# Performance work log

Hardware: AMD Instinct MI355X
Metric: run time of the kernel (lower is better)

Reference implementation:

```python
import jax, jax.numpy as jnp
import numpy as np

MAX_REL = 2  # hard-coded max_relative_position in the torch module


def setup_inputs() -> dict:
    key = jax.random.key(0)
    ks = jax.random.split(key, 12)
    B, S, Dm, H = 2, 2048, 1024, 16
    D = Dm // H
    sc = 1.0 / np.sqrt(Dm)
    inp = {
        "x": jax.random.normal(ks[0], (B, S, Dm), jnp.float32),
        "Wq": jax.random.normal(ks[1], (Dm, Dm), jnp.float32) * sc,
        "bq": jnp.zeros((Dm,), jnp.float32),
        "Wk": jax.random.normal(ks[2], (Dm, Dm), jnp.float32) * sc,
        "bk": jnp.zeros((Dm,), jnp.float32),
        "Wv": jax.random.normal(ks[3], (Dm, Dm), jnp.float32) * sc,
        "bv": jnp.zeros((Dm,), jnp.float32),
        "Wo": jax.random.normal(ks[4], (Dm, Dm), jnp.float32) * sc,
        "bo": jnp.zeros((Dm,), jnp.float32),
        "rel_k": jax.random.normal(ks[5], (2 * MAX_REL + 1, D), jnp.float32) * 0.1,
        "rel_v": jax.random.normal(ks[6], (2 * MAX_REL + 1, D), jnp.float32) * 0.1,
        "num_heads": H,
    }
    return inp


def reference(x, Wq, bq, Wk, bk, Wv, bv, Wo, bo, rel_k, rel_v, num_heads):
    B, S, Dm = x.shape
    H = num_heads
    D = Dm // H
    n_buckets = 2 * MAX_REL + 1

    q = (x @ Wq + bq).reshape(B, S, H, D).transpose(0, 2, 1, 3)  # [B,H,S,D]
    k = (x @ Wk + bk).reshape(B, S, H, D).transpose(0, 2, 1, 3)
    v = (x @ Wv + bv).reshape(B, S, H, D).transpose(0, 2, 1, 3)

    # content-content scores
    attn1 = jnp.einsum('bhqd,bhkd->bhqk', q, k)

    # relative-position bucket index: clip(k - q, -MAX_REL, MAX_REL) + MAX_REL
    r = jnp.arange(S)
    idx = jnp.clip(r[None, :] - r[:, None], -MAX_REL, MAX_REL) + MAX_REL  # [S,S] int

    # content-position scores: q . rel_k[idx]  (project onto 5 buckets then gather)
    q_rel = jnp.einsum('bhqd,jd->bhqj', q, rel_k)  # [B,H,S,5]
    attn2 = jnp.take_along_axis(q_rel, jnp.broadcast_to(idx[None, None], (B, H, S, S)), axis=-1)

    scores = (attn1 + attn2) / jnp.sqrt(jnp.asarray(D, x.dtype))
    p = jax.nn.softmax(scores, axis=-1)  # dropout in eval mode -> identity

    out1 = jnp.einsum('bhqk,bhkd->bhqd', p, v)

    # position value term: sum_k p[...,k] * rel_v[idx[q,k]] via bucket accumulation
    onehot = (idx[:, :, None] == jnp.arange(n_buckets)[None, None, :]).astype(p.dtype)  # [S,S,5]
    bucket = jnp.einsum('bhqk,qkj->bhqj', p, onehot)
    out2 = jnp.einsum('bhqj,jd->bhqd', bucket, rel_v)

    out = (out1 + out2).transpose(0, 2, 1, 3).reshape(B, S, Dm)
    return out @ Wo + bo
```

## Files before the change

kernel.cpp:

```cpp
#include <hip/hip_runtime.h>

#define S_LEN 2048
#define DM    1024
#define NH    16
#define HD    64
#define BATCH 2

typedef __attribute__((ext_vector_type(8))) short short8;
typedef __attribute__((ext_vector_type(4))) float f32x4;

__device__ inline float b2f(unsigned short u) {
    return __uint_as_float(((unsigned)u) << 16);
}
__device__ inline unsigned short f2b(float f) {
    unsigned u = __float_as_uint(f);
    u += 0x7FFFu + ((u >> 16) & 1u);
    return (unsigned short)(u >> 16);
}
__device__ inline f32x4 zero4() {
    f32x4 z; z[0] = 0.f; z[1] = 0.f; z[2] = 0.f; z[3] = 0.f; return z;
}

__device__ inline size_t qk_frag_idx(int s, int d) {
    return (size_t)(s >> 4) * 1024 + (size_t)(d >> 5) * 512
         + (size_t)(((d & 31) >> 3) * 16 + (s & 15)) * 8 + (d & 7);
}
__device__ inline size_t v_frag_idx(int s, int d) {
    return (size_t)(s >> 5) * 2048 + (size_t)(d >> 4) * 512
         + (size_t)(((s & 31) >> 3) * 16 + (d & 15)) * 8 + (s & 7);
}
__device__ inline size_t af_idx(int m, int k) {
    return ((size_t)(m >> 4) * 32 + (size_t)(k >> 5)) * 512
         + (size_t)(((k & 31) >> 3) * 16 + (m & 15)) * 8 + (k & 7);
}

__global__ __launch_bounds__(256) void convert_w(
    const float* __restrict__ Wq, const float* __restrict__ Wk,
    const float* __restrict__ Wv, const float* __restrict__ Wo,
    unsigned short* __restrict__ Wf)
{
    int k = blockIdx.x, mat = blockIdx.y, tid = threadIdx.x;
    const float* W = (mat == 0) ? Wq : (mat == 1) ? Wk : (mat == 2) ? Wv : Wo;
    f32x4 w = *(const f32x4*)(W + (size_t)k * DM + tid * 4);
    unsigned short* dst = Wf + ((size_t)mat << 20);
#pragma unroll
    for (int e = 0; e < 4; e++) dst[af_idx(tid * 4 + e, k)] = f2b(w[e]);
}

__global__ __launch_bounds__(256) void convert_x(
    const float* __restrict__ x, unsigned short* __restrict__ Xf, int b)
{
    int m = blockIdx.x, tid = threadIdx.x;
    f32x4 v = *(const f32x4*)(x + ((size_t)b * S_LEN + m) * DM + tid * 4);
#pragma unroll
    for (int e = 0; e < 4; e++) Xf[af_idx(m, tid * 4 + e)] = f2b(v[e]);
}

__global__ __launch_bounds__(256) void proj_gemm_wf(
    const unsigned short* __restrict__ Xf,
    const unsigned short* __restrict__ Wf,
    const float* __restrict__ bq, const float* __restrict__ bk,
    const float* __restrict__ bv,
    unsigned short* __restrict__ Qs, unsigned short* __restrict__ Ks,
    unsigned short* __restrict__ Vts)
{
    int tid = threadIdx.x;
    int wave = tid >> 6, lane = tid & 63;
    int r = lane & 15, quad = lane >> 4;
    int mat = blockIdx.y >> 4;
    int hh  = blockIdx.y & 15;

    int mt0 = blockIdx.x * 8 + wave * 2;
    const unsigned short* A0 = Xf + (size_t)mt0 * 32 * 512 + lane * 8;
    const unsigned short* A1 = A0 + 32 * 512;
    const unsigned short* Bb = Wf + ((size_t)mat << 20)
                             + (size_t)(hh * 4) * 32 * 512 + lane * 8;

    f32x4 acc[2][4];
#pragma unroll
    for (int mt = 0; mt < 2; mt++)
#pragma unroll
        for (int nt = 0; nt < 4; nt++) acc[mt][nt] = zero4();

    short8 a0c = *(const short8*)A0;
    short8 a1c = *(const short8*)A1;
    short8 b0c = *(const short8*)(Bb);
    short8 b1c = *(const short8*)(Bb + 16384);
    short8 b2c = *(const short8*)(Bb + 32768);
    short8 b3c = *(const short8*)(Bb + 49152);

    for (int kt = 0; kt < 32; kt++) {
        short8 a0n, a1n, b0n, b1n, b2n, b3n;
        if (kt < 31) {
            size_t off = (size_t)(kt + 1) * 512;
            a0n = *(const short8*)(A0 + off);
            a1n = *(const short8*)(A1 + off);
            b0n = *(const short8*)(Bb + off);
            b1n = *(const short8*)(Bb + 16384 + off);
            b2n = *(const short8*)(Bb + 32768 + off);
            b3n = *(const short8*)(Bb + 49152 + off);
        }
        acc[0][0] = __builtin_amdgcn_mfma_f32_16x16x32_bf16(a0c, b0c, acc[0][0], 0, 0, 0);
        acc[0][1] = __builtin_amdgcn_mfma_f32_16x16x32_bf16(a0c, b1c, acc[0][1], 0, 0, 0);
        acc[0][2] = __builtin_amdgcn_mfma_f32_16x16x32_bf16(a0c, b2c, acc[0][2], 0, 0, 0);
        acc[0][3] = __builtin_amdgcn_mfma_f32_16x16x32_bf16(a0c, b3c, acc[0][3], 0, 0, 0);
        acc[1][0] = __builtin_amdgcn_mfma_f32_16x16x32_bf16(a1c, b0c, acc[1][0], 0, 0, 0);
        acc[1][1] = __builtin_amdgcn_mfma_f32_16x16x32_bf16(a1c, b1c, acc[1][1], 0, 0, 0);
        acc[1][2] = __builtin_amdgcn_mfma_f32_16x16x32_bf16(a1c, b2c, acc[1][2], 0, 0, 0);
        acc[1][3] = __builtin_amdgcn_mfma_f32_16x16x32_bf16(a1c, b3c, acc[1][3], 0, 0, 0);
        a0c = a0n; a1c = a1n;
        b0c = b0n; b1c = b1n; b2c = b2n; b3c = b3n;
    }

    const float* bias = (mat == 0) ? bq : (mat == 1) ? bk : bv;
    size_t hbase = (size_t)hh * S_LEN * HD;
    int gc0 = hh * 64;
#pragma unroll
    for (int mt = 0; mt < 2; mt++) {
#pragma unroll
        for (int nt = 0; nt < 4; nt++) {
            int d = nt * 16 + r;
            float bb = bias[gc0 + d];
#pragma unroll
            for (int i = 0; i < 4; i++) {
                int s = blockIdx.x * 128 + wave * 32 + mt * 16 + quad * 4 + i;
                float v = acc[mt][nt][i] + bb;
                if (mat == 2)      Vts[hbase + v_frag_idx(s, d)] = f2b(v);
                else if (mat == 0) Qs [hbase + qk_frag_idx(s, d)] = f2b(v);
                else               Ks [hbase + qk_frag_idx(s, d)] = f2b(v);
            }
        }
    }
}

__global__ __launch_bounds__(256) void outproj_wf(
    const unsigned short* __restrict__ AOf,
    const unsigned short* __restrict__ Wof,
    const float* __restrict__ bo,
    float* __restrict__ out, int b)
{
    int tid = threadIdx.x;
    int wave = tid >> 6, lane = tid & 63;
    int r = lane & 15, quad = lane >> 4;

    int mt0 = blockIdx.x * 8 + wave * 2;
    const unsigned short* A0 = AOf + (size_t)mt0 * 32 * 512 + lane * 8;
    const unsigned short* A1 = A0 + 32 * 512;
    const unsigned short* Bb = Wof + (size_t)(blockIdx.y * 4) * 32 * 512 + lane * 8;

    f32x4 acc[2][4];
#pragma unroll
    for (int mt = 0; mt < 2; mt++)
#pragma unroll
        for (int nt = 0; nt < 4; nt++) acc[mt][nt] = zero4();

    short8 a0c = *(const short8*)A0;
    short8 a1c = *(const short8*)A1;
    short8 b0c = *(const short8*)(Bb);
    short8 b1c = *(const short8*)(Bb + 16384);
    short8 b2c = *(const short8*)(Bb + 32768);
    short8 b3c = *(const short8*)(Bb + 49152);

    for (int kt = 0; kt < 32; kt++) {
        short8 a0n, a1n, b0n, b1n, b2n, b3n;
        if (kt < 31) {
            size_t off = (size_t)(kt + 1) * 512;
            a0n = *(const short8*)(A0 + off);
            a1n = *(const short8*)(A1 + off);
            b0n = *(const short8*)(Bb + off);
            b1n = *(const short8*)(Bb + 16384 + off);
            b2n = *(const short8*)(Bb + 32768 + off);
            b3n = *(const short8*)(Bb + 49152 + off);
        }
        acc[0][0] = __builtin_amdgcn_mfma_f32_16x16x32_bf16(a0c, b0c, acc[0][0], 0, 0, 0);
        acc[0][1] = __builtin_amdgcn_mfma_f32_16x16x32_bf16(a0c, b1c, acc[0][1], 0, 0, 0);
        acc[0][2] = __builtin_amdgcn_mfma_f32_16x16x32_bf16(a0c, b2c, acc[0][2], 0, 0, 0);
        acc[0][3] = __builtin_amdgcn_mfma_f32_16x16x32_bf16(a0c, b3c, acc[0][3], 0, 0, 0);
        acc[1][0] = __builtin_amdgcn_mfma_f32_16x16x32_bf16(a1c, b0c, acc[1][0], 0, 0, 0);
        acc[1][1] = __builtin_amdgcn_mfma_f32_16x16x32_bf16(a1c, b1c, acc[1][1], 0, 0, 0);
        acc[1][2] = __builtin_amdgcn_mfma_f32_16x16x32_bf16(a1c, b2c, acc[1][2], 0, 0, 0);
        acc[1][3] = __builtin_amdgcn_mfma_f32_16x16x32_bf16(a1c, b3c, acc[1][3], 0, 0, 0);
        a0c = a0n; a1c = a1n;
        b0c = b0n; b1c = b1n; b2c = b2n; b3c = b3n;
    }

#pragma unroll
    for (int mt = 0; mt < 2; mt++) {
#pragma unroll
        for (int nt = 0; nt < 4; nt++) {
            int n = blockIdx.y * 64 + nt * 16 + r;
            float bb = bo[n];
#pragma unroll
            for (int i = 0; i < 4; i++) {
                int m = blockIdx.x * 128 + wave * 32 + mt * 16 + quad * 4 + i;
                out[((size_t)b * S_LEN + m) * DM + n] = acc[mt][nt][i] + bb;
            }
        }
    }
}

__global__ __launch_bounds__(256) void proj_fused_xf(
    const unsigned short* __restrict__ Xf,
    const float* __restrict__ Wq, const float* __restrict__ Wk,
    const float* __restrict__ Wv,
    const float* __restrict__ bq, const float* __restrict__ bk,
    const float* __restrict__ bv,
    unsigned short* __restrict__ Qs, unsigned short* __restrict__ Ks,
    unsigned short* __restrict__ Vts)
{
    __shared__ unsigned short Bs[64][72];

    int tid = threadIdx.x;
    int wave = tid >> 6, lane = tid & 63;
    int r = lane & 15, quad = lane >> 4;
    int m0 = blockIdx.x * 64 + wave * 16;
    int mat = blockIdx.y / NH;
    int hh  = blockIdx.y % NH;
    int gc0 = hh * 64;

    const float* W    = (mat == 0) ? Wq : (mat == 1) ? Wk : Wv;
    const float* bias = (mat == 0) ? bq : (mat == 1) ? bk : bv;

    f32x4 acc[4];
#pragma unroll
    for (int nt = 0; nt < 4; nt++) acc[nt] = zero4();

    int kr = tid >> 2;
    int nc = (tid & 3) * 16;
    const unsigned short* Af = Xf + (size_t)(blockIdx.x * 4 + wave) * 32 * 512 + lane * 8;

    for (int k0 = 0; k0 < DM; k0 += 64) {
        const f32x4* wr = (const f32x4*)(W + (size_t)(k0 + kr) * DM + gc0 + nc);
        f32x4 w0 = wr[0], w1 = wr[1], w2 = wr[2], w3 = wr[3];
        __syncthreads();
        Bs[nc +  0][kr] = f2b(w0[0]); Bs[nc +  1][kr] = f2b(w0[1]);
        Bs[nc +  2][kr] = f2b(w0[2]); Bs[nc +  3][kr] = f2b(w0[3]);
        Bs[nc +  4][kr] = f2b(w1[0]); Bs[nc +  5][kr] = f2b(w1[1]);
        Bs[nc +  6][kr] = f2b(w1[2]); Bs[nc +  7][kr] = f2b(w1[3]);
        Bs[nc +  8][kr] = f2b(w2[0]); Bs[nc +  9][kr] = f2b(w2[1]);
        Bs[nc + 10][kr] = f2b(w2[2]); Bs[nc + 11][kr] = f2b(w2[3]);
        Bs[nc + 12][kr] = f2b(w3[0]); Bs[nc + 13][kr] = f2b(w3[1]);
        Bs[nc + 14][kr] = f2b(w3[2]); Bs[nc + 15][kr] = f2b(w3[3]);
        __syncthreads();

#pragma unroll
        for (int ks = 0; ks < 2; ks++) {
            int kt = (k0 >> 5) + ks;
            short8 a = *(const short8*)(Af + (size_t)kt * 512);
#pragma unroll
            for (int nt = 0; nt < 4; nt++) {
                short8 bf = *(const short8*)&Bs[nt * 16 + r][ks * 32 + quad * 8];
                acc[nt] = __builtin_amdgcn_mfma_f32_16x16x32_bf16(a, bf, acc[nt], 0, 0, 0);
            }
        }
    }

    size_t hbase = (size_t)hh * S_LEN * HD;
#pragma unroll
    for (int nt = 0; nt < 4; nt++) {
        int d = nt * 16 + r;
        float bb = bias[gc0 + d];
#pragma unroll
        for (int i = 0; i < 4; i++) {
            int s = m0 + quad * 4 + i;
            float v = acc[nt][i] + bb;
            if (mat == 2)      Vts[hbase + v_frag_idx(s, d)] = f2b(v);
            else if (mat == 0) Qs [hbase + qk_frag_idx(s, d)] = f2b(v);
            else               Ks [hbase + qk_frag_idx(s, d)] = f2b(v);
        }
    }
}

__global__ __launch_bounds__(256) void proj_fused_legacy(
    const float* __restrict__ x,
    const float* __restrict__ Wq, const float* __restrict__ Wk,
    const float* __restrict__ Wv,
    const float* __restrict__ bq, const float* __restrict__ bk,
    const float* __restrict__ bv,
    unsigned short* __restrict__ Qs, unsigned short* __restrict__ Ks,
    unsigned short* __restrict__ Vts,
    int b, int head0, int NG)
{
    __shared__ unsigned short Bs[64][72];

    int tid = threadIdx.x;
    int wave = tid >> 6, lane = tid & 63;
    int r = lane & 15, quad = lane >> 4;
    int m0 = blockIdx.x * 64 + wave * 16;
    int mat = blockIdx.y / NG;
    int hh  = blockIdx.y % NG;
    int gc0 = (head0 + hh) * 64;

    const float* W    = (mat == 0) ? Wq : (mat == 1) ? Wk : Wv;
    const float* bias = (mat == 0) ? bq : (mat == 1) ? bk : bv;
    const float* xb = x + (size_t)b * S_LEN * DM;

    f32x4 acc[4];
#pragma unroll
    for (int nt = 0; nt < 4; nt++) acc[nt] = zero4();

    int kr = tid >> 2;
    int nc = (tid & 3) * 16;
    const float* am = xb + (size_t)(m0 + r) * DM + quad * 8;

    for (int k0 = 0; k0 < DM; k0 += 64) {
        const f32x4* wr = (const f32x4*)(W + (size_t)(k0 + kr) * DM + gc0 + nc);
        f32x4 w0 = wr[0], w1 = wr[1], w2 = wr[2], w3 = wr[3];
        __syncthreads();
        Bs[nc +  0][kr] = f2b(w0[0]); Bs[nc +  1][kr] = f2b(w0[1]);
        Bs[nc +  2][kr] = f2b(w0[2]); Bs[nc +  3][kr] = f2b(w0[3]);
        Bs[nc +  4][kr] = f2b(w1[0]); Bs[nc +  5][kr] = f2b(w1[1]);
        Bs[nc +  6][kr] = f2b(w1[2]); Bs[nc +  7][kr] = f2b(w1[3]);
        Bs[nc +  8][kr] = f2b(w2[0]); Bs[nc +  9][kr] = f2b(w2[1]);
        Bs[nc + 10][kr] = f2b(w2[2]); Bs[nc + 11][kr] = f2b(w2[3]);
        Bs[nc + 12][kr] = f2b(w3[0]); Bs[nc + 13][kr] = f2b(w3[1]);
        Bs[nc + 14][kr] = f2b(w3[2]); Bs[nc + 15][kr] = f2b(w3[3]);
        __syncthreads();

#pragma unroll
        for (int ks = 0; ks < 2; ks++) {
            const f32x4* ap = (const f32x4*)(am + k0 + ks * 32);
            f32x4 a0 = ap[0], a1 = ap[1];
            short8 a;
            a[0] = (short)f2b(a0[0]); a[1] = (short)f2b(a0[1]);
            a[2] = (short)f2b(a0[2]); a[3] = (short)f2b(a0[3]);
            a[4] = (short)f2b(a1[0]); a[5] = (short)f2b(a1[1]);
            a[6] = (short)f2b(a1[2]); a[7] = (short)f2b(a1[3]);
#pragma unroll
            for (int nt = 0; nt < 4; nt++) {
                short8 bf = *(const short8*)&Bs[nt * 16 + r][ks * 32 + quad * 8];
                acc[nt] = __builtin_amdgcn_mfma_f32_16x16x32_bf16(a, bf, acc[nt], 0, 0, 0);
            }
        }
    }

    size_t hbase = (size_t)hh * S_LEN * HD;
#pragma unroll
    for (int nt = 0; nt < 4; nt++) {
        int d = nt * 16 + r;
        float bb = bias[gc0 + d];
#pragma unroll
        for (int i = 0; i < 4; i++) {
            int s = m0 + quad * 4 + i;
            float v = acc[nt][i] + bb;
            if (mat == 2)      Vts[hbase + v_frag_idx(s, d)] = f2b(v);
            else if (mat == 0) Qs [hbase + qk_frag_idx(s, d)] = f2b(v);
            else               Ks [hbase + qk_frag_idx(s, d)] = f2b(v);
        }
    }
}

#define QK_TILE(T, EE)                                                        \
    {                                                                         \
        short8 bk0 = *(const short8*)(kb + (size_t)(T) * 1024);               \
        short8 bk1 = *(const short8*)(kb + (size_t)(T) * 1024 + 512);         \
        f32x4 sACC = zero4();                                                 \
        sACC = __builtin_amdgcn_mfma_f32_16x16x32_bf16(bk0, aq0, sACC, 0, 0, 0); \
        sACC = __builtin_amdgcn_mfma_f32_16x16x32_bf16(bk1, aq1, sACC, 0, 0, 0); \
        int c0 = wave * 128 + (T) * 16;                                       \
        bool below = (c0 + 17 <= q0);                                         \
        bool above = (c0 >= q0 + 17);                                         \
        if (below || above) {                                                 \
            float qsel = above ? qhi : qlo;                                   \
            float ts = 0.f;                                                   \
            _Pragma("unroll")                                                 \
            for (int i = 0; i < 4; i++) {                                     \
                float e = __builtin_amdgcn_exp2f(__fmaf_rn(sACC[i], C, qsel)); \
                EE[i] = e; ts += e;                                           \
            }                                                                 \
            dpart += ts;                                                      \
            if (above) spart += ts;                                           \
        } else {                                                              \
            _Pragma("unroll")                                                 \
            for (int i = 0; i < 4; i++) {                                     \
                int col = c0 + quad * 4 + i;                                  \
                int del = min(2, max(-2, col - qglob));                       \
                float e = __builtin_amdgcn_exp2f((sACC[i] + qrel_s[r][del + 2]) * C); \
                EE[i] = e; dpart += e;                                        \
                if (col >= qglob + 2) spart += e;                             \
                int dd = col - qglob;                                         \
                if (dd >= -1 && dd <= 1) diag_s[r][dd + 1] = e;               \
            }                                                                 \
        }                                                                     \
    }

__global__ __launch_bounds__(1024, 8) void attn_mfma(
    const unsigned short* __restrict__ Q,
    const unsigned short* __restrict__ Km,
    const unsigned short* __restrict__ Vt,
    const float* __restrict__ relk,
    const float* __restrict__ relv,
    unsigned short* __restrict__ Aout,
    int col_base,
    int NG, int ao_frag)
{
    __shared__ float obuf[16][16][66];
    __shared__ float qrel_s[16][5];
    __shared__ float relv_s[5][HD];
    __shared__ float rowstat[16][8];
    __shared__ float wden[16][16];
    __shared__ float wsuf[16][16];
    __shared__ float diag_s[16][4];

    int tid = threadIdx.x;
    int wave = tid >> 6, lane = tid & 63;
    int r = lane & 15, quad = lane >> 4;

    int bid = blockIdx.x;
    int hh, jq;
    if (NG == 16) {
        int xcd = bid & 7, j = bid >> 3;
        hh = xcd + ((j >> 7) << 3);
        jq = j & 127;
    } else {
        hh = bid >> 7;
        jq = bid & 127;
    }
    int q0 = jq << 4;

    size_t qk_base = (size_t)hh * S_LEN * HD;

    const unsigned short* qf = Q + qk_base + (size_t)(q0 >> 4) * 1024 + lane * 8;
    short8 aq0 = *(const short8*)qf;
    short8 aq1 = *(const short8*)(qf + 512);

    if (tid >= 384 && tid < 448) diag_s[(tid - 384) >> 2][(tid - 384) & 3] = 0.f;
    {
        int t2 = tid - 64;
        if (t2 >= 0 && t2 < 5 * HD) relv_s[t2 >> 6][t2 & 63] = relv[t2];
    }

    if (wave == 0) {
#pragma unroll
        for (int j = 0; j < 5; j++) {
            const f32x4* rk0 = (const f32x4*)(relk + j * HD + quad * 8);
            const f32x4* rk1 = (const f32x4*)(relk + j * HD + 32 + quad * 8);
            f32x4 r0a = rk0[0], r0b = rk0[1], r1a = rk1[0], r1b = rk1[1];
            float s = 0.f;
#pragma unroll
            for (int e = 0; e < 4; e++) {
                s += b2f((unsigned short)aq0[e])     * r0a[e];
                s += b2f((unsigned short)aq0[e + 4]) * r0b[e];
                s += b2f((unsigned short)aq1[e])     * r1a[e];
                s += b2f((unsigned short)aq1[e + 4]) * r1b[e];
            }
            s += __shfl_xor(s, 16);
            s += __shfl_xor(s, 32);
            if (quad == 0) qrel_s[r][j] = s;
        }
    }

    __syncthreads();

    const float C = 0.18033688f;
    float dpart = 0.f, spart = 0.f;
    float qlo = qrel_s[r][0] * C;
    float qhi = qrel_s[r][4] * C;
    int qglob = q0 + r;

    f32x4 oacc[4];
#pragma unroll
    for (int nt = 0; nt < 4; nt++) oacc[nt] = zero4();

    const unsigned short* kb = Km + qk_base + (size_t)(wave * 8) * 1024 + lane * 8;
    const unsigned short* vb = Vt + qk_base + (size_t)(wave * 4) * 2048 + lane * 8;

#pragma unroll 1
    for (int u = 0; u < 4; u++) {
        float e0[4], e1[4];
        QK_TILE(u * 2,     e0);
        QK_TILE(u * 2 + 1, e1);

        unsigned Au, Bu, Cu, Du;
        asm("v_cvt_pk_bf16_f32 %0, %1, %2" : "=v"(Au) : "v"(e0[0]), "v"(e0[1]));
        asm("v_cvt_pk_bf16_f32 %0, %1, %2" : "=v"(Bu) : "v"(e0[2]), "v"(e0[3]));
        asm("v_cvt_pk_bf16_f32 %0, %1, %2" : "=v"(Cu) : "v"(e1[0]), "v"(e1[1]));
        asm("v_cvt_pk_bf16_f32 %0, %1, %2" : "=v"(Du) : "v"(e1[2]), "v"(e1[3]));
        unsigned A2 = __shfl_xor(Au, 32), B2 = __shfl_xor(Bu, 32);
        unsigned C2 = __shfl_xor(Cu, 32), D2 = __shfl_xor(Du, 32);
        bool low = (lane < 32);
        unsigned M  = low ? Au : C2, N  = low ? Bu : D2;
        unsigned P  = low ? A2 : Cu, Qw = low ? B2 : Du;
        unsigned M2 = __shfl_xor(M, 16), N2 = __shfl_xor(N, 16);
        unsigned P2 = __shfl_xor(P, 16), Q2 = __shfl_xor(Qw, 16);
        bool even = ((lane & 16) == 0);
        union { unsigned u32[4]; short8 s8; } pa;
        pa.u32[0] = even ? M  : P2;
        pa.u32[1] = even ? N  : Q2;
        pa.u32[2] = even ? M2 : P;
        pa.u32[3] = even ? N2 : Qw;

        const unsigned short* vc = vb + (size_t)u * 2048;
#pragma unroll
        for (int nt = 0; nt < 4; nt++) {
            short8 bv = *(const short8*)(vc + (size_t)nt * 512);
            oacc[nt] = __builtin_amdgcn_mfma_f32_16x16x32_bf16(pa.s8, bv, oacc[nt], 0, 0, 0);
        }
    }

    dpart += __shfl_xor(dpart, 16); dpart += __shfl_xor(dpart, 32);
    spart += __shfl_xor(spart, 16); spart += __shfl_xor(spart, 32);
    if (lane < 16) { wden[wave][r] = dpart; wsuf[wave][r] = spart; }

#pragma unroll
    for (int nt = 0; nt < 4; nt++)
#pragma unroll
        for (int i = 0; i < 4; i++)
            obuf[wave][quad * 4 + i][nt * 16 + r] = oacc[nt][i];
    __syncthreads();

    if (tid < 16) {
        int row = tid;
        float denom = 0.f, suf = 0.f;
        for (int w = 0; w < 16; w++) { denom += wden[w][row]; suf += wsuf[w][row]; }
        float b1  = diag_s[row][0];
        float b2v = diag_s[row][1];
        float b3  = diag_s[row][2];
        rowstat[row][0] = 1.f / denom;
        rowstat[row][1] = denom - suf - b1 - b2v - b3;
        rowstat[row][2] = b1;
        rowstat[row][3] = b2v;
        rowstat[row][4] = b3;
        rowstat[row][5] = suf;
    }
    __syncthreads();

    {
        int orow = tid >> 6, ocol = tid & 63;
        float o = 0.f;
#pragma unroll
        for (int w = 0; w < 16; w++) o += obuf[w][orow][ocol];
        float o2 = rowstat[orow][1] * relv_s[0][ocol]
                 + rowstat[orow][2] * relv_s[1][ocol]
                 + rowstat[orow][3] * relv_s[2][ocol]
                 + rowstat[orow][4] * relv_s[3][ocol]
                 + rowstat[orow][5] * relv_s[4][ocol];
        float res = (o + o2) * rowstat[orow][0];
        int col = col_base + hh * HD + ocol;
        if (ao_frag)
            Aout[af_idx(q0 + orow, col)] = f2b(res);
        else
            Aout[(size_t)(q0 + orow) * DM + col] = f2b(res);
    }
}

__global__ __launch_bounds__(256) void outproj_fused(
    const unsigned short* __restrict__ AO,
    const float* __restrict__ Wo,
    const float* __restrict__ bo,
    float* __restrict__ out, int b)
{
    __shared__ unsigned short Bs[64][72];

    int tid = threadIdx.x;
    int wave = tid >> 6, lane = tid & 63;
    int r = lane & 15, quad = lane >> 4;
    int m0 = blockIdx.x * 64 + wave * 16;
    int n0 = blockIdx.y * 64;

    f32x4 acc[4];
#pragma unroll
    for (int nt = 0; nt < 4; nt++) acc[nt] = zero4();

    int kr = tid >> 2;
    int nc = (tid & 3) * 16;
    const short8* ap = (const short8*)(AO + (size_t)(m0 + r) * DM + quad * 8);

    for (int k0 = 0; k0 < DM; k0 += 64) {
        const f32x4* wr = (const f32x4*)(Wo + (size_t)(k0 + kr) * DM + n0 + nc);
        f32x4 w0 = wr[0], w1 = wr[1], w2 = wr[2], w3 = wr[3];
        __syncthreads();
        Bs[nc +  0][kr] = f2b(w0[0]); Bs[nc +  1][kr] = f2b(w0[1]);
        Bs[nc +  2][kr] = f2b(w0[2]); Bs[nc +  3][kr] = f2b(w0[3]);
        Bs[nc +  4][kr] = f2b(w1[0]); Bs[nc +  5][kr] = f2b(w1[1]);
        Bs[nc +  6][kr] = f2b(w1[2]); Bs[nc +  7][kr] = f2b(w1[3]);
        Bs[nc +  8][kr] = f2b(w2[0]); Bs[nc +  9][kr] = f2b(w2[1]);
        Bs[nc + 10][kr] = f2b(w2[2]); Bs[nc + 11][kr] = f2b(w2[3]);
        Bs[nc + 12][kr] = f2b(w3[0]); Bs[nc + 13][kr] = f2b(w3[1]);
        Bs[nc + 14][kr] = f2b(w3[2]); Bs[nc + 15][kr] = f2b(w3[3]);
        __syncthreads();

#pragma unroll
        for (int ks = 0; ks < 2; ks++) {
            short8 a = ap[ks * 4];
#pragma unroll
            for (int nt = 0; nt < 4; nt++) {
                short8 bf = *(const short8*)&Bs[nt * 16 + r][ks * 32 + quad * 8];
                acc[nt] = __builtin_amdgcn_mfma_f32_16x16x32_bf16(a, bf, acc[nt], 0, 0, 0);
            }
        }
        ap += 8;
    }

#pragma unroll
    for (int nt = 0; nt < 4; nt++) {
        int n = n0 + nt * 16 + r;
        float bb = bo[n];
#pragma unroll
        for (int i = 0; i < 4; i++) {
            int m = m0 + quad * 4 + i;
            out[((size_t)b * S_LEN + m) * DM + n] = acc[nt][i] + bb;
        }
    }
}

extern "C" void kernel_launch(void* const* d_in, const int* in_sizes, int n_in,
                              void* d_out, int out_size, void* d_ws, size_t ws_size,
                              hipStream_t stream)
{
    const float* x  = (const float*)d_in[0];
    const float* Wq = (const float*)d_in[1];
    const float* bq = (const float*)d_in[2];
    const float* Wk = (const float*)d_in[3];
    const float* bk = (const float*)d_in[4];
    const float* Wv = (const float*)d_in[5];
    const float* bv = (const float*)d_in[6];
    const float* Wo = (const float*)d_in[7];
    const float* bo = (const float*)d_in[8];
    const float* rk = (const float*)d_in[9];
    const float* rv = (const float*)d_in[10];
    float* outp = (float*)d_out;

    unsigned short* ws = (unsigned short*)d_ws;
    const size_t M1 = 1048576;

    if (ws_size >= (size_t)25165824) {
        unsigned short* Wf   = ws;
        unsigned short* XfAO = ws + 4 * M1;
        unsigned short* Qs   = ws + 6 * M1;
        unsigned short* Ks   = ws + 8 * M1;
        unsigned short* Vts  = ws + 10 * M1;

        convert_w<<<dim3(1024, 4), 256, 0, stream>>>(Wq, Wk, Wv, Wo, Wf);
        for (int b = 0; b < BATCH; b++) {
            convert_x<<<dim3(2048), 256, 0, stream>>>(x, XfAO, b);
            proj_gemm_wf<<<dim3(16, 48), 256, 0, stream>>>(
                XfAO, Wf, bq, bk, bv, Qs, Ks, Vts);
            attn_mfma<<<dim3(2048), 1024, 0, stream>>>(
                Qs, Ks, Vts, rk, rv, XfAO, 0, 16, 1);
            outproj_wf<<<dim3(16, 16), 256, 0, stream>>>(
                XfAO, Wf + 3 * M1, bo, outp, b);
        }
    } else if (ws_size >= (size_t)16777216) {
        unsigned short* XfAO = ws;
        unsigned short* Qs   = ws + 2 * M1;
        unsigned short* Ks   = ws + 4 * M1;
        unsigned short* Vts  = ws + 6 * M1;

        for (int b = 0; b < BATCH; b++) {
            convert_x<<<dim3(2048), 256, 0, stream>>>(x, XfAO, b);
            proj_fused_xf<<<dim3(32, 48), 256, 0, stream>>>(
                XfAO, Wq, Wk, Wv, bq, bk, bv, Qs, Ks, Vts);
            attn_mfma<<<dim3(2048), 1024, 0, stream>>>(
                Qs, Ks, Vts, rk, rv, XfAO, 0, 16, 0);
            outproj_fused<<<dim3(32, 16), 256, 0, stream>>>(XfAO, Wo, bo, outp, b);
        }
    } else {
        const int NG = 4;
        const size_t slice = (size_t)NG * S_LEN * HD;
        unsigned short* Qs  = ws;
        unsigned short* Ks  = ws + slice;
        unsigned short* Vts = ws + 2 * slice;
        unsigned short* AOb = ws + 3 * slice;

        for (int b = 0; b < BATCH; b++) {
            for (int g = 0; g < NH / NG; g++) {
                int head0 = g * NG;
                proj_fused_legacy<<<dim3(32, 3 * NG), 256, 0, stream>>>(
                    x, Wq, Wk, Wv, bq, bk, bv, Qs, Ks, Vts, b, head0, NG);
                attn_mfma<<<dim3((S_LEN / 16) * NG), 1024, 0, stream>>>(
                    Qs, Ks, Vts, rk, rv, AOb, head0 * HD, NG, 0);
            }
            outproj_fused<<<dim3(32, 16), 256, 0, stream>>>(AOb, Wo, bo, outp, b);
        }
    }
}
```

Measured before the change: 310.3 us.

## Process 64 query rows per attention block with 4 key chunks per wave group

The attention kernel now covers 64 query rows per block instead of 16. The 16 waves split into 4 query tiles by 4 key chunks, and each wave loops over 512 keys instead of 128. This cuts the grid from 2048 to 512 blocks and amortises the per-block setup, the relv and qrel loads and the final reduction over four times as many rows. The cost is fewer blocks in flight and a longer serial loop per wave, which may reduce latency hiding. Each wave also no longer shares its K tiles with the other query tiles, so K and V are read more times from cache.

```diff
diff --git a/kernel.cpp b/kernel.cpp
--- a/kernel.cpp
+++ b/kernel.cpp
@@ -357,9 +357,9 @@
         f32x4 sACC = zero4();                                                 \
         sACC = __builtin_amdgcn_mfma_f32_16x16x32_bf16(bk0, aq0, sACC, 0, 0, 0); \
         sACC = __builtin_amdgcn_mfma_f32_16x16x32_bf16(bk1, aq1, sACC, 0, 0, 0); \
-        int c0 = wave * 128 + (T) * 16;                                       \
-        bool below = (c0 + 17 <= q0);                                         \
-        bool above = (c0 >= q0 + 17);                                         \
+        int c0 = kc * 512 + (T) * 16;                                         \
+        bool below = (c0 + 17 <= qbase);                                      \
+        bool above = (c0 >= qbase + 17);                                      \
         if (below || above) {                                                 \
             float qsel = above ? qhi : qlo;                                   \
             float ts = 0.f;                                                   \
@@ -375,11 +375,11 @@
             for (int i = 0; i < 4; i++) {                                     \
                 int col = c0 + quad * 4 + i;                                  \
                 int del = min(2, max(-2, col - qglob));                       \
-                float e = __builtin_amdgcn_exp2f((sACC[i] + qrel_s[r][del + 2]) * C); \
+                float e = __builtin_amdgcn_exp2f((sACC[i] + qrel_s[rloc][del + 2]) * C); \
                 EE[i] = e; dpart += e;                                        \
                 if (col >= qglob + 2) spart += e;                             \
                 int dd = col - qglob;                                         \
-                if (dd >= -1 && dd <= 1) diag_s[r][dd + 1] = e;               \
+                if (dd >= -1 && dd <= 1) diag_s[rloc][dd + 1] = e;            \
             }                                                                 \
         }                                                                     \
     }
@@ -395,42 +395,45 @@
     int NG, int ao_frag)
 {
     __shared__ float obuf[16][16][66];
-    __shared__ float qrel_s[16][5];
+    __shared__ float qrel_s[64][5];
     __shared__ float relv_s[5][HD];
-    __shared__ float rowstat[16][8];
+    __shared__ float rowstat[64][8];
     __shared__ float wden[16][16];
     __shared__ float wsuf[16][16];
-    __shared__ float diag_s[16][4];
+    __shared__ float diag_s[64][4];
 
     int tid = threadIdx.x;
     int wave = tid >> 6, lane = tid & 63;
     int r = lane & 15, quad = lane >> 4;
+    int qt = wave >> 2, kc = wave & 3;
 
     int bid = blockIdx.x;
     int hh, jq;
     if (NG == 16) {
         int xcd = bid & 7, j = bid >> 3;
-        hh = xcd + ((j >> 7) << 3);
-        jq = j & 127;
+        hh = xcd + ((j >> 5) << 3);
+        jq = j & 31;
     } else {
-        hh = bid >> 7;
-        jq = bid & 127;
-    }
-    int q0 = jq << 4;
+        hh = bid >> 5;
+        jq = bid & 31;
+    }
+    int q0 = jq << 6;
+    int qbase = q0 + qt * 16;
+    int rloc = qt * 16 + r;
 
     size_t qk_base = (size_t)hh * S_LEN * HD;
 
-    const unsigned short* qf = Q + qk_base + (size_t)(q0 >> 4) * 1024 + lane * 8;
+    const unsigned short* qf = Q + qk_base + (size_t)((q0 >> 4) + qt) * 1024 + lane * 8;
     short8 aq0 = *(const short8*)qf;
     short8 aq1 = *(const short8*)(qf + 512);
 
-    if (tid >= 384 && tid < 448) diag_s[(tid - 384) >> 2][(tid - 384) & 3] = 0.f;
+    if (tid >= 384 && tid < 640) ((float*)diag_s)[tid - 384] = 0.f;
     {
         int t2 = tid - 64;
         if (t2 >= 0 && t2 < 5 * HD) relv_s[t2 >> 6][t2 & 63] = relv[t2];
     }
 
-    if (wave == 0) {
+    if (kc == 0) {
 #pragma unroll
         for (int j = 0; j < 5; j++) {
             const f32x4* rk0 = (const f32x4*)(relk + j * HD + quad * 8);
@@ -446,7 +449,7 @@
             }
             s += __shfl_xor(s, 16);
             s += __shfl_xor(s, 32);
-            if (quad == 0) qrel_s[r][j] = s;
+            if (quad == 0) qrel_s[rloc][j] = s;
         }
     }
 
@@ -454,19 +457,19 @@
 
     const float C = 0.18033688f;
     float dpart = 0.f, spart = 0.f;
-    float qlo = qrel_s[r][0] * C;
-    float qhi = qrel_s[r][4] * C;
-    int qglob = q0 + r;
+    float qlo = qrel_s[rloc][0] * C;
+    float qhi = qrel_s[rloc][4] * C;
+    int qglob = qbase + r;
 
     f32x4 oacc[4];
 #pragma unroll
     for (int nt = 0; nt < 4; nt++) oacc[nt] = zero4();
 
-    const unsigned short* kb = Km + qk_base + (size_t)(wave * 8) * 1024 + lane * 8;
-    const unsigned short* vb = Vt + qk_base + (size_t)(wave * 4) * 2048 + lane * 8;
+    const unsigned short* kb = Km + qk_base + (size_t)(kc * 32) * 1024 + lane * 8;
+    const unsigned short* vb = Vt + qk_base + (size_t)(kc * 16) * 2048 + lane * 8;
 
 #pragma unroll 1
-    for (int u = 0; u < 4; u++) {
+    for (int u = 0; u < 16; u++) {
         float e0[4], e1[4];
         QK_TILE(u * 2,     e0);
         QK_TILE(u * 2 + 1, e1);
@@ -509,10 +512,15 @@
             obuf[wave][quad * 4 + i][nt * 16 + r] = oacc[nt][i];
     __syncthreads();
 
-    if (tid < 16) {
+    if (tid < 64) {
         int row = tid;
+        int qt2 = row >> 4, lr = row & 15;
         float denom = 0.f, suf = 0.f;
-        for (int w = 0; w < 16; w++) { denom += wden[w][row]; suf += wsuf[w][row]; }
+#pragma unroll
+        for (int w = 0; w < 4; w++) {
+            denom += wden[qt2 * 4 + w][lr];
+            suf   += wsuf[qt2 * 4 + w][lr];
+        }
         float b1  = diag_s[row][0];
         float b2v = diag_s[row][1];
         float b3  = diag_s[row][2];
@@ -526,21 +534,24 @@
     __syncthreads();
 
     {
-        int orow = tid >> 6, ocol = tid & 63;
-        float o = 0.f;
-#pragma unroll
-        for (int w = 0; w < 16; w++) o += obuf[w][orow][ocol];
-        float o2 = rowstat[orow][1] * relv_s[0][ocol]
-                 + rowstat[orow][2] * relv_s[1][ocol]
-                 + rowstat[orow][3] * relv_s[2][ocol]
-                 + rowstat[orow][4] * relv_s[3][ocol]
-                 + rowstat[orow][5] * relv_s[4][ocol];
-        float res = (o + o2) * rowstat[orow][0];
-        int col = col_base + hh * HD + ocol;
-        if (ao_frag)
-            Aout[af_idx(q0 + orow, col)] = f2b(res);
-        else
-            Aout[(size_t)(q0 + orow) * DM + col] = f2b(res);
+        int lr = tid >> 6, ocol = tid & 63;
+#pragma unroll
+        for (int it = 0; it < 4; it++) {
+            int R = it * 16 + lr;
+            float o = obuf[it * 4 + 0][lr][ocol] + obuf[it * 4 + 1][lr][ocol]
+                    + obuf[it * 4 + 2][lr][ocol] + obuf[it * 4 + 3][lr][ocol];
+            float o2 = rowstat[R][1] * relv_s[0][ocol]
+                     + rowstat[R][2] * relv_s[1][ocol]
+                     + rowstat[R][3] * relv_s[2][ocol]
+                     + rowstat[R][4] * relv_s[3][ocol]
+                     + rowstat[R][5] * relv_s[4][ocol];
+            float res = (o + o2) * rowstat[R][0];
+            int col = col_base + hh * HD + ocol;
+            if (ao_frag)
+                Aout[af_idx(q0 + R, col)] = f2b(res);
+            else
+                Aout[(size_t)(q0 + R) * DM + col] = f2b(res);
+        }
     }
 }
 
@@ -636,7 +647,7 @@
             convert_x<<<dim3(2048), 256, 0, stream>>>(x, XfAO, b);
             proj_gemm_wf<<<dim3(16, 48), 256, 0, stream>>>(
                 XfAO, Wf, bq, bk, bv, Qs, Ks, Vts);
-            attn_mfma<<<dim3(2048), 1024, 0, stream>>>(
+            attn_mfma<<<dim3(512), 1024, 0, stream>>>(
                 Qs, Ks, Vts, rk, rv, XfAO, 0, 16, 1);
             outproj_wf<<<dim3(16, 16), 256, 0, stream>>>(
                 XfAO, Wf + 3 * M1, bo, outp, b);
@@ -651,7 +662,7 @@
             convert_x<<<dim3(2048), 256, 0, stream>>>(x, XfAO, b);
             proj_fused_xf<<<dim3(32, 48), 256, 0, stream>>>(
                 XfAO, Wq, Wk, Wv, bq, bk, bv, Qs, Ks, Vts);
-            attn_mfma<<<dim3(2048), 1024, 0, stream>>>(
+            attn_mfma<<<dim3(512), 1024, 0, stream>>>(
                 Qs, Ks, Vts, rk, rv, XfAO, 0, 16, 0);
             outproj_fused<<<dim3(32, 16), 256, 0, stream>>>(XfAO, Wo, bo, outp, b);
         }
@@ -668,7 +679,7 @@
                 int head0 = g * NG;
                 proj_fused_legacy<<<dim3(32, 3 * NG), 256, 0, stream>>>(
                     x, Wq, Wk, Wv, bq, bk, bv, Qs, Ks, Vts, b, head0, NG);
-                attn_mfma<<<dim3((S_LEN / 16) * NG), 1024, 0, stream>>>(
+                attn_mfma<<<dim3(32 * NG), 1024, 0, stream>>>(
                     Qs, Ks, Vts, rk, rv, AOb, head0 * HD, NG, 0);
             }
             outproj_fused<<<dim3(32, 16), 256, 0, stream>>>(AOb, Wo, bo, outp, b);
```

Result: faster. 291.9 us (-5.9%).
